# Optimization experiments

Hardware: AMD Instinct MI355X
Metric: run time of the kernel (lower is better)

Reference implementation:

```python
import jax, jax.numpy as jnp
import numpy as np

NUM_USERS = 50000
NUM_ITEMS = 50000
NUM_NODES = NUM_USERS + NUM_ITEMS
EMB_DIM = 128
NUM_LAYERS = 3
NUM_EDGES = 2000000
AVG_DEG = NUM_EDGES / NUM_NODES  # ~20, used to normalize edge weights


def setup_inputs() -> dict:
    key = jax.random.key(0)
    k1, k2, k3, k4 = jax.random.split(key, 4)
    # Xavier-uniform-ish embedding init
    emb_weight = jax.random.normal(k1, (NUM_NODES, EMB_DIM), dtype=jnp.float32) * (1.0 / np.sqrt(EMB_DIM))
    rows = jax.random.randint(k2, (NUM_EDGES,), 0, NUM_NODES, dtype=jnp.int32)
    cols = jax.random.randint(k3, (NUM_EDGES,), 0, NUM_NODES, dtype=jnp.int32)
    # positive normalized edge weights, ~1/deg so spectral radius stays ~1
    vals = jax.random.uniform(k4, (NUM_EDGES,), dtype=jnp.float32) * jnp.float32(2.0 / AVG_DEG)
    return {"emb_weight": emb_weight, "rows": rows, "cols": cols, "vals": vals}


def reference(emb_weight, rows, cols, vals):
    # LightGCN.get_user_item_emb(): multi-layer SpMM propagation + layer mean.
    N = emb_weight.shape[0]

    def spmm(x):
        # out[r] += vals[e] * x[cols[e]] for each edge e with rows[e] == r
        return jax.ops.segment_sum(vals[:, None] * x[cols], rows, num_segments=N)

    x = emb_weight
    acc = x  # running sum of layer outputs (fused stack+mean)
    for _ in range(NUM_LAYERS):
        x = spmm(x)
        acc = acc + x
    x_final = acc / jnp.float32(NUM_LAYERS + 1)
    user_emb = x_final[:NUM_USERS]
    item_emb = x_final[NUM_USERS:]
    return user_emb, item_emb
```

## Files before the change

### kernel.cpp

```cpp
#include <hip/hip_runtime.h>
#include <hip/hip_fp16.h>


#define DIM  128
#define PB   256
#define KPAD 512
#define RPB  256
#define NSCAN (KPAD * PB)
#define NTILES (NSCAN / 1024)
#define PCAP 7168

static inline size_t align_up(size_t v, size_t a) { return (v + a - 1) & ~(a - 1); }

union H2 { unsigned u; __half2 h; };

__global__ void __launch_bounds__(1024)
lgcn_prep(const float2* __restrict__ emb2, int* __restrict__ x0q,
          float* __restrict__ sc0, int n,
          const int* __restrict__ rows, int* __restrict__ ghist, int nedges,
          unsigned long long* __restrict__ tstat) {
    __shared__ int h[KPAD];
    const int b = blockIdx.x, tid = threadIdx.x;
    if (b < PB) {
        for (int k = tid; k < KPAD; k += 1024) h[k] = 0;
        __syncthreads();
        const int chunk = (nedges + PB - 1) / PB;
        const int beg = b * chunk;
        const int end = min(beg + chunk, nedges);
        for (int e = beg + tid; e < end; e += 1024)
            atomicAdd(&h[rows[e] >> 8], 1);
        __syncthreads();
        for (int k = tid; k < KPAD; k += 1024) ghist[(k << 8) + b] = h[k];
    } else if (b == PB) {
        if (tid < NTILES) tstat[tid] = 0ull;
    } else {
        const int wid  = tid >> 6;
        const int lane = tid & 63;
        const int row  = (b - PB - 1) * 16 + wid;
        if (row >= n) return;
        float2 v = emb2[(size_t)row * 64 + lane];
        float m = fmaxf(fabsf(v.x), fabsf(v.y));
        #pragma unroll
        for (int off = 1; off < 64; off <<= 1)
            m = fmaxf(m, __shfl_xor(m, off));
        const float inv = 127.0f / fmaxf(m, 1e-20f);
        int q0 = (int)(v.x * inv + 128.5f);
        int q1 = (int)(v.y * inv + 128.5f);
        q0 = min(max(q0, 0), 255); q1 = min(max(q1, 0), 255);
        ((unsigned short*)x0q)[(size_t)row * 64 + lane] =
            (unsigned short)(q0 | (q1 << 8));
        if (lane == 0) sc0[row] = m * (1.0f / 127.0f);
    }
}

__global__ void __launch_bounds__(256)
lgcn_scan(const int* __restrict__ ghist, int* __restrict__ gbase,
          unsigned long long* __restrict__ tstat, int nscan) {
    __shared__ int wsum[4];
    __shared__ int btot_s, prev_s;
    const int tile = blockIdx.x;
    const int tid  = threadIdx.x;
    const int lane = tid & 63;
    const int wid  = tid >> 6;
    const int i0   = tile * 1024 + tid * 4;

    int4 c = *(const int4*)(ghist + i0);
    const int t1 = c.x + c.y, t2 = t1 + c.z, tsum = t2 + c.w;

    int incl = tsum;
    #pragma unroll
    for (int off = 1; off < 64; off <<= 1) {
        int t = __shfl_up(incl, off, 64);
        if (lane >= off) incl += t;
    }
    if (lane == 63) wsum[wid] = incl;
    __syncthreads();
    int woff = 0;
    #pragma unroll
    for (int w = 0; w < 4; ++w) woff += (w < wid) ? wsum[w] : 0;
    const int ex = woff + incl - tsum;
    if (tid == 255) btot_s = woff + incl;
    __syncthreads();
    const int btot = btot_s;

    if (tile == 0) {
        if (tid == 0) {
            __hip_atomic_store(&tstat[0],
                (((unsigned long long)(unsigned)btot) << 32) | 2ull,
                __ATOMIC_RELEASE, __HIP_MEMORY_SCOPE_AGENT);
            prev_s = 0;
        }
    } else if (wid == 0) {
        if (lane == 0)
            __hip_atomic_store(&tstat[tile],
                (((unsigned long long)(unsigned)btot) << 32) | 1ull,
                __ATOMIC_RELEASE, __HIP_MEMORY_SCOPE_AGENT);
        int run = 0;
        int base_p = tile - 1;
        while (true) {
            const int p = base_p - lane;
            unsigned long long st;
            if (p >= 0) {
                do {
                    st = __hip_atomic_load(&tstat[p],
                        __ATOMIC_ACQUIRE, __HIP_MEMORY_SCOPE_AGENT);
                    if (((unsigned)st & 3u) != 0u) break;
                    __builtin_amdgcn_s_sleep(1);
                } while (true);
            } else {
                st = 2ull;
            }
            const unsigned f = (unsigned)st & 3u;
            const int v = (int)(unsigned)(st >> 32);
            const unsigned long long inc_mask = __ballot(f == 2u);
            int contrib;
            if (inc_mask != 0ull) {
                const int l_star = (int)(__ffsll((long long)inc_mask) - 1);
                contrib = (lane <= l_star) ? v : 0;
            } else {
                contrib = v;
            }
            #pragma unroll
            for (int off = 1; off < 64; off <<= 1)
                contrib += __shfl_xor(contrib, off);
            run += contrib;
            if (inc_mask != 0ull) break;
            base_p -= 64;
        }
        if (lane == 0) {
            __hip_atomic_store(&tstat[tile],
                (((unsigned long long)(unsigned)(run + btot)) << 32) | 2ull,
                __ATOMIC_RELEASE, __HIP_MEMORY_SCOPE_AGENT);
            prev_s = run;
        }
    }
    __syncthreads();
    const int pv = prev_s;

    int4 o;
    o.x = pv + ex;
    o.y = pv + ex + c.x;
    o.z = pv + ex + t1;
    o.w = pv + ex + t2;
    *(int4*)(gbase + i0) = o;
    if (tile == gridDim.x - 1 && tid == 255) gbase[nscan] = pv + btot;
}

__global__ void __launch_bounds__(1024)
lgcn_part(const int* __restrict__ rows, const int* __restrict__ cols,
          const float* __restrict__ vals, const int* __restrict__ gbase,
          int2* __restrict__ staging, int nedges) {
    __shared__ int lcnt[KPAD];
    const int b = blockIdx.x, tid = threadIdx.x;
    for (int k = tid; k < KPAD; k += 1024) lcnt[k] = gbase[(k << 8) + b];
    __syncthreads();
    const int chunk = (nedges + PB - 1) / PB;
    const int beg = b * chunk;
    const int end = min(beg + chunk, nedges);
    for (int e = beg + tid; e < end; e += 1024) {
        int r   = rows[e];
        int pos = atomicAdd(&lcnt[r >> 8], 1);
        staging[pos] = make_int2(cols[e] | ((r & 255) << 17),
                                 __float_as_int(vals[e] * 256.0f));
    }
}

__global__ void __launch_bounds__(1024)
lgcn_place(const int* __restrict__ gbase, const int2* __restrict__ staging,
           int* __restrict__ row_ptr, int2* __restrict__ edges, int n, int nbuck) {
    __shared__ int rcnt[RPB];
    __shared__ int cur[RPB];
    __shared__ int wsum[4];
    __shared__ int2 cache[PCAP];
    const int k    = blockIdx.x;
    const int tid  = threadIdx.x;
    const int base = gbase[k << 8];
    const int next = gbase[(k + 1) << 8];
    const int cnt  = next - base;
    const bool fit = (cnt <= PCAP);

    if (tid < RPB) rcnt[tid] = 0;
    __syncthreads();
    if (fit) {
        for (int i = tid; i < cnt; i += 1024) {
            int2 p = staging[base + i];
            cache[i] = p;
            atomicAdd(&rcnt[(p.x >> 17) & 255], 1);
        }
    } else {
        for (int i = base + tid; i < next; i += 1024)
            atomicAdd(&rcnt[(staging[i].x >> 17) & 255], 1);
    }
    __syncthreads();

    if (tid < RPB) {
        const int lane = tid & 63;
        const int wid  = tid >> 6;
        const int v = rcnt[tid];
        int incl = v;
        #pragma unroll
        for (int off = 1; off < 64; off <<= 1) {
            int t = __shfl_up(incl, off, 64);
            if (lane >= off) incl += t;
        }
        if (lane == 63) wsum[wid] = incl;
        __syncthreads();
        int woff = 0;
        #pragma unroll
        for (int w = 0; w < 4; ++w) woff += (w < wid) ? wsum[w] : 0;
        const int ex = woff + incl - v;

        cur[tid] = base + ex;
        const int r = (k << 8) + tid;
        if (r < n) row_ptr[r] = base + ex;
        if (k == nbuck - 1 && tid == 0) row_ptr[n] = next;
    } else {
        __syncthreads();
    }
    __syncthreads();

    if (fit) {
        for (int i = tid; i < cnt; i += 1024) {
            int2 p  = cache[i];
            int pos = atomicAdd(&cur[(p.x >> 17) & 255], 1);
            edges[pos] = make_int2(p.x & 0x1FFFF, p.y);
        }
    } else {
        for (int i = base + tid; i < next; i += 1024) {
            int2 p  = staging[i];
            int pos = atomicAdd(&cur[(p.x >> 17) & 255], 1);
            edges[pos] = make_int2(p.x & 0x1FFFF, p.y);
        }
    }
}

__global__ void __launch_bounds__(256)
lgcn_spmm(const int* __restrict__ row_ptr, const int2* __restrict__ edges,
          const int2* __restrict__ xq, const float* __restrict__ scin,
          int2* __restrict__ xqout, float* __restrict__ scout,
          const float2* __restrict__ emb, const int2* __restrict__ x1q,
          const float* __restrict__ sc1, float2* __restrict__ out,
          int n, int mode) {
    const int wave = blockIdx.x * 4 + (threadIdx.x >> 6);
    const int lane = threadIdx.x & 63;
    const int g    = lane >> 4;
    const int l    = lane & 15;
    if (wave >= n) return;
    const int beg = row_ptr[wave];
    const int end = row_ptr[wave + 1];

    H2 A0, A1, A2, A3;
    A0.u = 0; A1.u = 0; A2.u = 0; A3.u = 0;
    H2 BIAS; BIAS.u = 0xE480E480;

#define QFMA8(QQ, SV)                                                         \
    {                                                                         \
        H2 hv; hv.h = __float2half2_rn(SV);                                   \
        H2 p;                                                                 \
        p.u = __builtin_amdgcn_perm(0x64646464u, (unsigned)(QQ).x, 0x05010400u); \
        A0.h = __hfma2(__hadd2(p.h, BIAS.h), hv.h, A0.h);                     \
        p.u = __builtin_amdgcn_perm(0x64646464u, (unsigned)(QQ).x, 0x05030402u); \
        A1.h = __hfma2(__hadd2(p.h, BIAS.h), hv.h, A1.h);                     \
        p.u = __builtin_amdgcn_perm(0x64646464u, (unsigned)(QQ).y, 0x05010400u); \
        A2.h = __hfma2(__hadd2(p.h, BIAS.h), hv.h, A2.h);                     \
        p.u = __builtin_amdgcn_perm(0x64646464u, (unsigned)(QQ).y, 0x05030402u); \
        A3.h = __hfma2(__hadd2(p.h, BIAS.h), hv.h, A3.h);                     \
    }

    int e = beg;
    for (; e + 16 <= end; e += 16) {
        int2 d0 = edges[e + g];
        int2 d1 = edges[e + 4 + g];
        int2 d2 = edges[e + 8 + g];
        int2 d3 = edges[e + 12 + g];
        float s0 = scin[d0.x], s1 = scin[d1.x], s2 = scin[d2.x], s3 = scin[d3.x];
        int2 q0 = xq[d0.x * 16 + l];
        int2 q1 = xq[d1.x * 16 + l];
        int2 q2 = xq[d2.x * 16 + l];
        int2 q3 = xq[d3.x * 16 + l];
        QFMA8(q0, s0 * __int_as_float(d0.y));
        QFMA8(q1, s1 * __int_as_float(d1.y));
        QFMA8(q2, s2 * __int_as_float(d2.y));
        QFMA8(q3, s3 * __int_as_float(d3.y));
    }
    for (; e + 8 <= end; e += 8) {
        int2 d0 = edges[e + g];
        int2 d1 = edges[e + 4 + g];
        float s0 = scin[d0.x], s1 = scin[d1.x];
        int2 q0 = xq[d0.x * 16 + l];
        int2 q1 = xq[d1.x * 16 + l];
        QFMA8(q0, s0 * __int_as_float(d0.y));
        QFMA8(q1, s1 * __int_as_float(d1.y));
    }
    for (; e < end; e += 4) {
        const int ee = e + g;
        int2 d = (ee < end) ? edges[ee] : make_int2(0, 0);
        float s = scin[d.x];
        int2 q = xq[d.x * 16 + l];
        QFMA8(q, s * __int_as_float(d.y));
    }
#undef QFMA8

    const float DS = 0.00390625f;
    float2 f0 = __half22float2(A0.h), f1 = __half22float2(A1.h);
    float2 f2 = __half22float2(A2.h), f3 = __half22float2(A3.h);
    float a0 = f0.x * DS, a1 = f0.y * DS, a2 = f1.x * DS, a3 = f1.y * DS;
    float a4 = f2.x * DS, a5 = f2.y * DS, a6 = f3.x * DS, a7 = f3.y * DS;

    a0 += __shfl_xor(a0, 16); a0 += __shfl_xor(a0, 32);
    a1 += __shfl_xor(a1, 16); a1 += __shfl_xor(a1, 32);
    a2 += __shfl_xor(a2, 16); a2 += __shfl_xor(a2, 32);
    a3 += __shfl_xor(a3, 16); a3 += __shfl_xor(a3, 32);
    a4 += __shfl_xor(a4, 16); a4 += __shfl_xor(a4, 32);
    a5 += __shfl_xor(a5, 16); a5 += __shfl_xor(a5, 32);
    a6 += __shfl_xor(a6, 16); a6 += __shfl_xor(a6, 32);
    a7 += __shfl_xor(a7, 16); a7 += __shfl_xor(a7, 32);

    if (mode == 0) {
        float m = fmaxf(fmaxf(fmaxf(fabsf(a0), fabsf(a1)), fmaxf(fabsf(a2), fabsf(a3))),
                        fmaxf(fmaxf(fabsf(a4), fabsf(a5)), fmaxf(fabsf(a6), fabsf(a7))));
        m = fmaxf(m, __shfl_xor(m, 1));
        m = fmaxf(m, __shfl_xor(m, 2));
        m = fmaxf(m, __shfl_xor(m, 4));
        m = fmaxf(m, __shfl_xor(m, 8));
        const float inv = 127.0f / fmaxf(m, 1e-20f);
        int q0 = min(max((int)(a0 * inv + 128.5f), 0), 255);
        int q1 = min(max((int)(a1 * inv + 128.5f), 0), 255);
        int q2 = min(max((int)(a2 * inv + 128.5f), 0), 255);
        int q3 = min(max((int)(a3 * inv + 128.5f), 0), 255);
        int q4 = min(max((int)(a4 * inv + 128.5f), 0), 255);
        int q5 = min(max((int)(a5 * inv + 128.5f), 0), 255);
        int q6 = min(max((int)(a6 * inv + 128.5f), 0), 255);
        int q7 = min(max((int)(a7 * inv + 128.5f), 0), 255);
        if (g == 0) {
            int2 r;
            r.x = q0 | (q1 << 8) | (q2 << 16) | (q3 << 24);
            r.y = q4 | (q5 << 8) | (q6 << 16) | (q7 << 24);
            xqout[wave * 16 + l] = r;
            if (l == 0) scout[wave] = m * (1.0f / 127.0f);
        }
    } else {
        if (g == 0) {
            float4 e0 = ((const float4*)emb)[wave * 32 + l * 2 + 0];
            float4 e1 = ((const float4*)emb)[wave * 32 + l * 2 + 1];
            int2 u1 = x1q[wave * 16 + l];
            int2 u2 = xq[wave * 16 + l];
            const float s1 = sc1[wave],  o1 = -128.0f * s1;
            const float s2 = scin[wave], o2 = -128.0f * s2;
            float b0 = fmaf((float)( u1.x        & 255), s1, o1);
            float b1 = fmaf((float)((u1.x >> 8)  & 255), s1, o1);
            float b2 = fmaf((float)((u1.x >> 16) & 255), s1, o1);
            float b3 = fmaf((float)((u1.x >> 24) & 255), s1, o1);
            float b4 = fmaf((float)( u1.y        & 255), s1, o1);
            float b5 = fmaf((float)((u1.y >> 8)  & 255), s1, o1);
            float b6 = fmaf((float)((u1.y >> 16) & 255), s1, o1);
            float b7 = fmaf((float)((u1.y >> 24) & 255), s1, o1);
            float c0 = fmaf((float)( u2.x        & 255), s2, o2);
            float c1 = fmaf((float)((u2.x >> 8)  & 255), s2, o2);
            float c2 = fmaf((float)((u2.x >> 16) & 255), s2, o2);
            float c3 = fmaf((float)((u2.x >> 24) & 255), s2, o2);
            float c4 = fmaf((float)( u2.y        & 255), s2, o2);
            float c5 = fmaf((float)((u2.y >> 8)  & 255), s2, o2);
            float c6 = fmaf((float)((u2.y >> 16) & 255), s2, o2);
            float c7 = fmaf((float)((u2.y >> 24) & 255), s2, o2);
            float4 r0, r1;
            r0.x = (e0.x + b0 + c0 + a0) * 0.25f;
            r0.y = (e0.y + b1 + c1 + a1) * 0.25f;
            r0.z = (e0.z + b2 + c2 + a2) * 0.25f;
            r0.w = (e0.w + b3 + c3 + a3) * 0.25f;
            r1.x = (e1.x + b4 + c4 + a4) * 0.25f;
            r1.y = (e1.y + b5 + c5 + a5) * 0.25f;
            r1.z = (e1.z + b6 + c6 + a6) * 0.25f;
            r1.w = (e1.w + b7 + c7 + a7) * 0.25f;
            ((float4*)out)[wave * 32 + l * 2 + 0] = r0;
            ((float4*)out)[wave * 32 + l * 2 + 1] = r1;
        }
    }
}

extern "C" void kernel_launch(void* const* d_in, const int* in_sizes, int n_in,
                              void* d_out, int out_size, void* d_ws, size_t ws_size,
                              hipStream_t stream) {
    const float* emb  = (const float*)d_in[0];
    const int*   rows = (const int*)d_in[1];
    const int*   cols = (const int*)d_in[2];
    const float* vals = (const float*)d_in[3];

    const int  n_nodes = in_sizes[0] / DIM;
    const int  nedges  = in_sizes[1];
    const long nd      = (long)n_nodes * DIM;

    char* ws = (char*)d_ws;
    size_t off = 0;
    int2* bufA    = (int2*)(ws + off); off = align_up(off + (size_t)nd, 256);
    int2* bufB    = (int2*)(ws + off); off = align_up(off + (size_t)nd, 256);
    int2* edges   = (int2*)(ws + off); off = align_up(off + (size_t)nedges * 8, 256);
    int2* staging = (int2*)(ws + off); off = align_up(off + (size_t)nedges * 8, 256);
    float* scA    = (float*)(ws + off); off = align_up(off + (size_t)n_nodes * 4, 256);
    float* scB    = (float*)(ws + off); off = align_up(off + (size_t)n_nodes * 4, 256);
    int* row_ptr  = (int*)(ws + off);  off = align_up(off + (size_t)(n_nodes + 1) * 4, 256);
    int* ghist    = (int*)(ws + off);  off = align_up(off + (size_t)NSCAN * 4, 256);
    int* gbase    = (int*)(ws + off);  off = align_up(off + ((size_t)NSCAN + 1) * 4, 256);
    unsigned long long* tstat = (unsigned long long*)(ws + off);
    off = align_up(off + (size_t)NTILES * 8, 256);
    float2* out   = (float2*)d_out;

    const int BS = 256;
    const int nbuck   = (n_nodes + RPB - 1) / RPB;
    const int grid_c  = (n_nodes + 15) / 16;
    const int grid_s  = (n_nodes + 3) / 4;

    lgcn_prep<<<PB + 1 + grid_c, 1024, 0, stream>>>((const float2*)emb, (int*)bufA,
                                                    scA, n_nodes, rows, ghist,
                                                    nedges, tstat);
    lgcn_scan<<<NTILES, BS, 0, stream>>>(ghist, gbase, tstat, NSCAN);
    lgcn_part<<<PB, 1024, 0, stream>>>(rows, cols, vals, gbase, staging, nedges);
    lgcn_place<<<nbuck, 1024, 0, stream>>>(gbase, staging, row_ptr, edges, n_nodes, nbuck);

    lgcn_spmm<<<grid_s, BS, 0, stream>>>(row_ptr, edges, bufA, scA, bufB, scB,
                                         nullptr, nullptr, nullptr, nullptr,
                                         n_nodes, 0);
    lgcn_spmm<<<grid_s, BS, 0, stream>>>(row_ptr, edges, bufB, scB, bufA, scA,
                                         nullptr, nullptr, nullptr, nullptr,
                                         n_nodes, 0);
    lgcn_spmm<<<grid_s, BS, 0, stream>>>(row_ptr, edges, bufA, scA, nullptr, nullptr,
                                         (const float2*)emb, bufB, scB, out,
                                         n_nodes, 1);
}
```

Measured before the change: 356.0 us.

## Fuse graph-build kernels into one persistent kernel with grid barriers

Merges the prep, scan, partition and place kernels into a single persistent 256-block kernel that separates phases with atomic grid-wide barriers. The decoupled-lookback scan becomes a two-level scan: per-tile scans, a single-block scan of tile sums, then an add pass. The goal is to remove the launch overheads and tail gaps between the build kernels. In exchange it adds five global barriers and depends on all 256 blocks of 1024 threads being co-resident; if they are not, the kernel deadlocks. It also loses parallelism in the quantize and place phases, since fixed blocks now loop over that work.

Measured after the change: 452.3 us. +27.1%, slower.

```diff
diff --git a/kernel.cpp b/kernel.cpp
--- a/kernel.cpp
+++ b/kernel.cpp
@@ -9,194 +9,76 @@
 #define NSCAN (KPAD * PB)
 #define NTILES (NSCAN / 1024)
 #define PCAP 7168
+#define NB   256
+#define NT   1024
 
 static inline size_t align_up(size_t v, size_t a) { return (v + a - 1) & ~(a - 1); }
 
 union H2 { unsigned u; __half2 h; };
 
+__device__ __forceinline__ void gbar(int* bar, int target) {
+    __syncthreads();
+    if (threadIdx.x == 0) {
+        __hip_atomic_fetch_add(bar, 1, __ATOMIC_ACQ_REL, __HIP_MEMORY_SCOPE_AGENT);
+        while (__hip_atomic_load(bar, __ATOMIC_ACQUIRE,
+                                 __HIP_MEMORY_SCOPE_AGENT) < target)
+            __builtin_amdgcn_s_sleep(2);
+    }
+    __syncthreads();
+}
+
 __global__ void __launch_bounds__(1024)
-lgcn_prep(const float2* __restrict__ emb2, int* __restrict__ x0q,
-          float* __restrict__ sc0, int n,
-          const int* __restrict__ rows, int* __restrict__ ghist, int nedges,
-          unsigned long long* __restrict__ tstat) {
-    __shared__ int h[KPAD];
-    const int b = blockIdx.x, tid = threadIdx.x;
-    if (b < PB) {
-        for (int k = tid; k < KPAD; k += 1024) h[k] = 0;
-        __syncthreads();
-        const int chunk = (nedges + PB - 1) / PB;
-        const int beg = b * chunk;
-        const int end = min(beg + chunk, nedges);
-        for (int e = beg + tid; e < end; e += 1024)
-            atomicAdd(&h[rows[e] >> 8], 1);
-        __syncthreads();
-        for (int k = tid; k < KPAD; k += 1024) ghist[(k << 8) + b] = h[k];
-    } else if (b == PB) {
-        if (tid < NTILES) tstat[tid] = 0ull;
-    } else {
-        const int wid  = tid >> 6;
-        const int lane = tid & 63;
-        const int row  = (b - PB - 1) * 16 + wid;
-        if (row >= n) return;
-        float2 v = emb2[(size_t)row * 64 + lane];
-        float m = fmaxf(fabsf(v.x), fabsf(v.y));
-        #pragma unroll
-        for (int off = 1; off < 64; off <<= 1)
-            m = fmaxf(m, __shfl_xor(m, off));
-        const float inv = 127.0f / fmaxf(m, 1e-20f);
-        int q0 = (int)(v.x * inv + 128.5f);
-        int q1 = (int)(v.y * inv + 128.5f);
-        q0 = min(max(q0, 0), 255); q1 = min(max(q1, 0), 255);
-        ((unsigned short*)x0q)[(size_t)row * 64 + lane] =
-            (unsigned short)(q0 | (q1 << 8));
-        if (lane == 0) sc0[row] = m * (1.0f / 127.0f);
-    }
-}
-
-__global__ void __launch_bounds__(256)
-lgcn_scan(const int* __restrict__ ghist, int* __restrict__ gbase,
-          unsigned long long* __restrict__ tstat, int nscan) {
-    __shared__ int wsum[4];
-    __shared__ int btot_s, prev_s;
-    const int tile = blockIdx.x;
+lgcn_build(const float2* __restrict__ emb2, int* __restrict__ x0q,
+           float* __restrict__ sc0, int n,
+           const int* __restrict__ rows, const int* __restrict__ cols,
+           const float* __restrict__ vals,
+           int* __restrict__ ghist, int* __restrict__ gbase,
+           int* __restrict__ bsums, int2* __restrict__ staging,
+           int2* __restrict__ edges, int* __restrict__ row_ptr,
+           int nedges, int nbuck, int* __restrict__ bar) {
+    __shared__ int2 cache[PCAP];
+    __shared__ int  hh[KPAD];
+    __shared__ int  rcnt[RPB];
+    __shared__ int  cur[RPB];
+    __shared__ int  wsum[16];
+    __shared__ int  wext[17];
+
+    const int b    = blockIdx.x;
     const int tid  = threadIdx.x;
     const int lane = tid & 63;
     const int wid  = tid >> 6;
-    const int i0   = tile * 1024 + tid * 4;
-
-    int4 c = *(const int4*)(ghist + i0);
-    const int t1 = c.x + c.y, t2 = t1 + c.z, tsum = t2 + c.w;
-
-    int incl = tsum;
-    #pragma unroll
-    for (int off = 1; off < 64; off <<= 1) {
-        int t = __shfl_up(incl, off, 64);
-        if (lane >= off) incl += t;
-    }
-    if (lane == 63) wsum[wid] = incl;
-    __syncthreads();
-    int woff = 0;
-    #pragma unroll
-    for (int w = 0; w < 4; ++w) woff += (w < wid) ? wsum[w] : 0;
-    const int ex = woff + incl - tsum;
-    if (tid == 255) btot_s = woff + incl;
-    __syncthreads();
-    const int btot = btot_s;
-
-    if (tile == 0) {
-        if (tid == 0) {
-            __hip_atomic_store(&tstat[0],
-                (((unsigned long long)(unsigned)btot) << 32) | 2ull,
-                __ATOMIC_RELEASE, __HIP_MEMORY_SCOPE_AGENT);
-            prev_s = 0;
-        }
-    } else if (wid == 0) {
-        if (lane == 0)
-            __hip_atomic_store(&tstat[tile],
-                (((unsigned long long)(unsigned)btot) << 32) | 1ull,
-                __ATOMIC_RELEASE, __HIP_MEMORY_SCOPE_AGENT);
-        int run = 0;
-        int base_p = tile - 1;
-        while (true) {
-            const int p = base_p - lane;
-            unsigned long long st;
-            if (p >= 0) {
-                do {
-                    st = __hip_atomic_load(&tstat[p],
-                        __ATOMIC_ACQUIRE, __HIP_MEMORY_SCOPE_AGENT);
-                    if (((unsigned)st & 3u) != 0u) break;
-                    __builtin_amdgcn_s_sleep(1);
-                } while (true);
-            } else {
-                st = 2ull;
-            }
-            const unsigned f = (unsigned)st & 3u;
-            const int v = (int)(unsigned)(st >> 32);
-            const unsigned long long inc_mask = __ballot(f == 2u);
-            int contrib;
-            if (inc_mask != 0ull) {
-                const int l_star = (int)(__ffsll((long long)inc_mask) - 1);
-                contrib = (lane <= l_star) ? v : 0;
-            } else {
-                contrib = v;
-            }
-            #pragma unroll
-            for (int off = 1; off < 64; off <<= 1)
-                contrib += __shfl_xor(contrib, off);
-            run += contrib;
-            if (inc_mask != 0ull) break;
-            base_p -= 64;
-        }
-        if (lane == 0) {
-            __hip_atomic_store(&tstat[tile],
-                (((unsigned long long)(unsigned)(run + btot)) << 32) | 2ull,
-                __ATOMIC_RELEASE, __HIP_MEMORY_SCOPE_AGENT);
-            prev_s = run;
-        }
-    }
-    __syncthreads();
-    const int pv = prev_s;
-
-    int4 o;
-    o.x = pv + ex;
-    o.y = pv + ex + c.x;
-    o.z = pv + ex + t1;
-    o.w = pv + ex + t2;
-    *(int4*)(gbase + i0) = o;
-    if (tile == gridDim.x - 1 && tid == 255) gbase[nscan] = pv + btot;
-}
-
-__global__ void __launch_bounds__(1024)
-lgcn_part(const int* __restrict__ rows, const int* __restrict__ cols,
-          const float* __restrict__ vals, const int* __restrict__ gbase,
-          int2* __restrict__ staging, int nedges) {
-    __shared__ int lcnt[KPAD];
-    const int b = blockIdx.x, tid = threadIdx.x;
-    for (int k = tid; k < KPAD; k += 1024) lcnt[k] = gbase[(k << 8) + b];
-    __syncthreads();
     const int chunk = (nedges + PB - 1) / PB;
     const int beg = b * chunk;
     const int end = min(beg + chunk, nedges);
-    for (int e = beg + tid; e < end; e += 1024) {
-        int r   = rows[e];
-        int pos = atomicAdd(&lcnt[r >> 8], 1);
-        staging[pos] = make_int2(cols[e] | ((r & 255) << 17),
-                                 __float_as_int(vals[e] * 256.0f));
-    }
-}
-
-__global__ void __launch_bounds__(1024)
-lgcn_place(const int* __restrict__ gbase, const int2* __restrict__ staging,
-           int* __restrict__ row_ptr, int2* __restrict__ edges, int n, int nbuck) {
-    __shared__ int rcnt[RPB];
-    __shared__ int cur[RPB];
-    __shared__ int wsum[4];
-    __shared__ int2 cache[PCAP];
-    const int k    = blockIdx.x;
-    const int tid  = threadIdx.x;
-    const int base = gbase[k << 8];
-    const int next = gbase[(k + 1) << 8];
-    const int cnt  = next - base;
-    const bool fit = (cnt <= PCAP);
-
-    if (tid < RPB) rcnt[tid] = 0;
-    __syncthreads();
-    if (fit) {
-        for (int i = tid; i < cnt; i += 1024) {
-            int2 p = staging[base + i];
-            cache[i] = p;
-            atomicAdd(&rcnt[(p.x >> 17) & 255], 1);
-        }
-    } else {
-        for (int i = base + tid; i < next; i += 1024)
-            atomicAdd(&rcnt[(staging[i].x >> 17) & 255], 1);
-    }
-    __syncthreads();
-
-    if (tid < RPB) {
-        const int lane = tid & 63;
-        const int wid  = tid >> 6;
-        const int v = rcnt[tid];
+
+    for (int k = tid; k < KPAD; k += NT) hh[k] = 0;
+    __syncthreads();
+    for (int e = beg + tid; e < end; e += NT)
+        atomicAdd(&hh[rows[e] >> 8], 1);
+    const int ngrp = (n + 15) >> 4;
+    for (int grp = b; grp < ngrp; grp += NB) {
+        const int row = grp * 16 + wid;
+        if (row < n) {
+            float2 v = emb2[(size_t)row * 64 + lane];
+            float m = fmaxf(fabsf(v.x), fabsf(v.y));
+            #pragma unroll
+            for (int off = 1; off < 64; off <<= 1)
+                m = fmaxf(m, __shfl_xor(m, off));
+            const float inv = 127.0f / fmaxf(m, 1e-20f);
+            int q0 = min(max((int)(v.x * inv + 128.5f), 0), 255);
+            int q1 = min(max((int)(v.y * inv + 128.5f), 0), 255);
+            ((unsigned short*)x0q)[(size_t)row * 64 + lane] =
+                (unsigned short)(q0 | (q1 << 8));
+            if (lane == 0) sc0[row] = m * (1.0f / 127.0f);
+        }
+    }
+    __syncthreads();
+    for (int k = tid; k < KPAD; k += NT) ghist[(k << 8) + b] = hh[k];
+    gbar(bar, NB * 1);
+
+    if (b < NTILES) {
+        const int i0 = b * 1024 + tid;
+        const int v = ghist[i0];
         int incl = v;
         #pragma unroll
         for (int off = 1; off < 64; off <<= 1) {
@@ -205,32 +87,107 @@
         }
         if (lane == 63) wsum[wid] = incl;
         __syncthreads();
-        int woff = 0;
+        if (tid == 0) {
+            int r = 0;
+            #pragma unroll
+            for (int w = 0; w < 16; ++w) { wext[w] = r; r += wsum[w]; }
+            wext[16] = r;
+        }
+        __syncthreads();
+        gbase[i0] = wext[wid] + incl - v;
+        if (tid == 0) bsums[b] = wext[16];
+    }
+    gbar(bar, NB * 2);
+
+    if (b == 0) {
+        int v = (tid < NTILES) ? bsums[tid] : 0;
+        int incl = v;
         #pragma unroll
-        for (int w = 0; w < 4; ++w) woff += (w < wid) ? wsum[w] : 0;
-        const int ex = woff + incl - v;
-
-        cur[tid] = base + ex;
-        const int r = (k << 8) + tid;
-        if (r < n) row_ptr[r] = base + ex;
-        if (k == nbuck - 1 && tid == 0) row_ptr[n] = next;
-    } else {
-        __syncthreads();
-    }
-    __syncthreads();
-
-    if (fit) {
-        for (int i = tid; i < cnt; i += 1024) {
-            int2 p  = cache[i];
-            int pos = atomicAdd(&cur[(p.x >> 17) & 255], 1);
-            edges[pos] = make_int2(p.x & 0x1FFFF, p.y);
-        }
-    } else {
-        for (int i = base + tid; i < next; i += 1024) {
-            int2 p  = staging[i];
-            int pos = atomicAdd(&cur[(p.x >> 17) & 255], 1);
-            edges[pos] = make_int2(p.x & 0x1FFFF, p.y);
-        }
+        for (int off = 1; off < 64; off <<= 1) {
+            int t = __shfl_up(incl, off, 64);
+            if (lane >= off) incl += t;
+        }
+        if (tid == 63) wsum[0] = incl;
+        __syncthreads();
+        if (tid < NTILES) {
+            const int ex = incl - v + ((wid == 1) ? wsum[0] : 0);
+            bsums[tid] = ex;
+            if (tid == NTILES - 1) gbase[NSCAN] = ex + v;
+        }
+    }
+    gbar(bar, NB * 3);
+
+    {
+        const int i = b * 1024 + tid;
+        if (i < NSCAN) gbase[i] += bsums[i >> 10];
+    }
+    gbar(bar, NB * 4);
+
+    for (int k = tid; k < KPAD; k += NT) hh[k] = gbase[(k << 8) + b];
+    __syncthreads();
+    for (int e = beg + tid; e < end; e += NT) {
+        int r   = rows[e];
+        int pos = atomicAdd(&hh[r >> 8], 1);
+        staging[pos] = make_int2(cols[e] | ((r & 255) << 17),
+                                 __float_as_int(vals[e] * 256.0f));
+    }
+    gbar(bar, NB * 5);
+
+    for (int k = b; k < nbuck; k += NB) {
+        const int base = gbase[k << 8];
+        const int next = gbase[(k + 1) << 8];
+        const int cnt  = next - base;
+        const bool fit = (cnt <= PCAP);
+
+        if (tid < RPB) rcnt[tid] = 0;
+        __syncthreads();
+        if (fit) {
+            for (int i = tid; i < cnt; i += NT) {
+                int2 p = staging[base + i];
+                cache[i] = p;
+                atomicAdd(&rcnt[(p.x >> 17) & 255], 1);
+            }
+        } else {
+            for (int i = base + tid; i < next; i += NT)
+                atomicAdd(&rcnt[(staging[i].x >> 17) & 255], 1);
+        }
+        __syncthreads();
+
+        int v = (tid < RPB) ? rcnt[tid] : 0;
+        int incl = v;
+        #pragma unroll
+        for (int off = 1; off < 64; off <<= 1) {
+            int t = __shfl_up(incl, off, 64);
+            if (lane >= off) incl += t;
+        }
+        if (wid < 4 && lane == 63) wsum[wid] = incl;
+        __syncthreads();
+        if (tid < RPB) {
+            int woff = 0;
+            #pragma unroll
+            for (int w = 0; w < 4; ++w) woff += (w < wid) ? wsum[w] : 0;
+            const int ex = woff + incl - v;
+            cur[tid] = base + ex;
+            const int r = (k << 8) + tid;
+            if (r < n) row_ptr[r] = base + ex;
+            if (k == nbuck - 1 && tid == 0) row_ptr[n] = next;
+        }
+        __syncthreads();
+
+        if (fit) {
+            for (int i = tid; i < cnt; i += NT) {
+                int2 p  = cache[i];
+                int pos = atomicAdd(&cur[(p.x >> 17) & 255], 1);
+                edges[pos] = make_int2(p.x & 0x1FFFF, p.y);
+            }
+        } else {
+            for (int i = base + tid; i < next; i += NT) {
+                int2 p  = staging[i];
+                int pos = atomicAdd(&cur[(p.x >> 17) & 255], 1);
+                edges[pos] = make_int2(p.x & 0x1FFFF, p.y);
+            }
+        }
+        __syncthreads();
     }
 }
 
@@ -401,21 +358,18 @@
     int* row_ptr  = (int*)(ws + off);  off = align_up(off + (size_t)(n_nodes + 1) * 4, 256);
     int* ghist    = (int*)(ws + off);  off = align_up(off + (size_t)NSCAN * 4, 256);
     int* gbase    = (int*)(ws + off);  off = align_up(off + ((size_t)NSCAN + 1) * 4, 256);
-    unsigned long long* tstat = (unsigned long long*)(ws + off);
-    off = align_up(off + (size_t)NTILES * 8, 256);
+    int* bsums    = (int*)(ws + off);  off = align_up(off + (size_t)NTILES * 4, 256);
+    int* bar      = (int*)(ws + off);  off = align_up(off + 256, 256);
     float2* out   = (float2*)d_out;
 
     const int BS = 256;
-    const int nbuck   = (n_nodes + RPB - 1) / RPB;
-    const int grid_c  = (n_nodes + 15) / 16;
-    const int grid_s  = (n_nodes + 3) / 4;
-
-    lgcn_prep<<<PB + 1 + grid_c, 1024, 0, stream>>>((const float2*)emb, (int*)bufA,
-                                                    scA, n_nodes, rows, ghist,
-                                                    nedges, tstat);
-    lgcn_scan<<<NTILES, BS, 0, stream>>>(ghist, gbase, tstat, NSCAN);
-    lgcn_part<<<PB, 1024, 0, stream>>>(rows, cols, vals, gbase, staging, nedges);
-    lgcn_place<<<nbuck, 1024, 0, stream>>>(gbase, staging, row_ptr, edges, n_nodes, nbuck);
+    const int nbuck  = (n_nodes + RPB - 1) / RPB;
+    const int grid_s = (n_nodes + 3) / 4;
+
+    hipMemsetAsync(bar, 0, sizeof(int), stream);
+    lgcn_build<<<NB, NT, 0, stream>>>((const float2*)emb, (int*)bufA, scA, n_nodes,
+                                      rows, cols, vals, ghist, gbase, bsums,
+                                      staging, edges, row_ptr, nedges, nbuck, bar);
 
     lgcn_spmm<<<grid_s, BS, 0, stream>>>(row_ptr, edges, bufA, scA, bufB, scB,
                                          nullptr, nullptr, nullptr, nullptr,
```

## Requantize embeddings to per-bucket scales held in LDS for SpMM gathers

Applied to the files above, without the earlier changes.

Adds a rescale pass that converts per-row int8 quantization scales into one shared scale per 256-row bucket, re-encoding each row's bytes. The SpMM kernel then loads all bucket scales into LDS and reads the gather scale from there instead of doing a random global load per edge. The first rescale is folded into the partition kernel as extra blocks, and SpMM moves to 1024-thread blocks. This adds two extra rescale launches and loses precision for rows whose magnitude is far below the bucket maximum.

New measurement: 408.7 us. 14.8% more time.

```diff
diff --git a/kernel.cpp b/kernel.cpp
--- a/kernel.cpp
+++ b/kernel.cpp
@@ -44,9 +44,8 @@
         for (int off = 1; off < 64; off <<= 1)
             m = fmaxf(m, __shfl_xor(m, off));
         const float inv = 127.0f / fmaxf(m, 1e-20f);
-        int q0 = (int)(v.x * inv + 128.5f);
-        int q1 = (int)(v.y * inv + 128.5f);
-        q0 = min(max(q0, 0), 255); q1 = min(max(q1, 0), 255);
+        int q0 = min(max((int)(v.x * inv + 128.5f), 0), 255);
+        int q1 = min(max((int)(v.y * inv + 128.5f), 0), 255);
         ((unsigned short*)x0q)[(size_t)row * 64 + lane] =
             (unsigned short)(q0 | (q1 << 8));
         if (lane == 0) sc0[row] = m * (1.0f / 127.0f);
@@ -146,22 +145,85 @@
     if (tile == gridDim.x - 1 && tid == 255) gbase[nscan] = pv + btot;
 }
 
+__device__ __forceinline__ void rescale_bucket(int k, int* __restrict__ xq,
+                                               const float* __restrict__ scR,
+                                               float* __restrict__ sB, int n,
+                                               float* srow, float* smax) {
+    const int tid = threadIdx.x;
+    const int rbeg = k << 8;
+    if (tid < RPB) {
+        int r = rbeg + tid;
+        srow[tid] = (r < n) ? scR[r] : 0.f;
+    }
+    __syncthreads();
+    if (tid < RPB) {
+        float v = srow[tid];
+        #pragma unroll
+        for (int off = 1; off < 64; off <<= 1) v = fmaxf(v, __shfl_xor(v, off));
+        if ((tid & 63) == 0) smax[tid >> 6] = v;
+    }
+    __syncthreads();
+    const float sBv = fmaxf(fmaxf(fmaxf(smax[0], smax[1]),
+                                  fmaxf(smax[2], smax[3])), 1e-20f);
+    if (tid == 0) sB[k] = sBv;
+    const int row = rbeg + (tid >> 2);
+    if (row >= n) return;
+    const float ratio = srow[tid >> 2] / sBv;
+    int4* p = (int4*)xq + (size_t)row * 8 + (size_t)(tid & 3) * 2;
+    #pragma unroll
+    for (int h = 0; h < 2; ++h) {
+        int4 v = p[h];
+        int r0 = v.x, r1 = v.y, r2 = v.z, r3 = v.w;
+        int o0 = 0, o1 = 0, o2 = 0, o3 = 0;
+        #pragma unroll
+        for (int byt = 0; byt < 4; ++byt) {
+            int b0 = (r0 >> (byt * 8)) & 255;
+            int b1 = (r1 >> (byt * 8)) & 255;
+            int b2 = (r2 >> (byt * 8)) & 255;
+            int b3 = (r3 >> (byt * 8)) & 255;
+            int n0 = min(max((int)(((float)b0 - 128.f) * ratio + 128.5f), 0), 255);
+            int n1 = min(max((int)(((float)b1 - 128.f) * ratio + 128.5f), 0), 255);
+            int n2 = min(max((int)(((float)b2 - 128.f) * ratio + 128.5f), 0), 255);
+            int n3 = min(max((int)(((float)b3 - 128.f) * ratio + 128.5f), 0), 255);
+            o0 |= n0 << (byt * 8); o1 |= n1 << (byt * 8);
+            o2 |= n2 << (byt * 8); o3 |= n3 << (byt * 8);
+        }
+        p[h] = make_int4(o0, o1, o2, o3);
+    }
+}
+
+__global__ void __launch_bounds__(1024)
+lgcn_rescale(int* __restrict__ xq, const float* __restrict__ scR,
+             float* __restrict__ sB, int n) {
+    __shared__ float srow[RPB];
+    __shared__ float smax[4];
+    rescale_bucket(blockIdx.x, xq, scR, sB, n, srow, smax);
+}
+
 __global__ void __launch_bounds__(1024)
 lgcn_part(const int* __restrict__ rows, const int* __restrict__ cols,
           const float* __restrict__ vals, const int* __restrict__ gbase,
-          int2* __restrict__ staging, int nedges) {
+          int2* __restrict__ staging, int nedges,
+          int* __restrict__ x0q, const float* __restrict__ scR,
+          float* __restrict__ sB0, int n) {
     __shared__ int lcnt[KPAD];
+    __shared__ float srow[RPB];
+    __shared__ float smax[4];
     const int b = blockIdx.x, tid = threadIdx.x;
-    for (int k = tid; k < KPAD; k += 1024) lcnt[k] = gbase[(k << 8) + b];
-    __syncthreads();
-    const int chunk = (nedges + PB - 1) / PB;
-    const int beg = b * chunk;
-    const int end = min(beg + chunk, nedges);
-    for (int e = beg + tid; e < end; e += 1024) {
-        int r   = rows[e];
-        int pos = atomicAdd(&lcnt[r >> 8], 1);
-        staging[pos] = make_int2(cols[e] | ((r & 255) << 17),
-                                 __float_as_int(vals[e] * 256.0f));
+    if (b < PB) {
+        for (int k = tid; k < KPAD; k += 1024) lcnt[k] = gbase[(k << 8) + b];
+        __syncthreads();
+        const int chunk = (nedges + PB - 1) / PB;
+        const int beg = b * chunk;
+        const int end = min(beg + chunk, nedges);
+        for (int e = beg + tid; e < end; e += 1024) {
+            int r   = rows[e];
+            int pos = atomicAdd(&lcnt[r >> 8], 1);
+            staging[pos] = make_int2(cols[e] | ((r & 255) << 17),
+                                     __float_as_int(vals[e] * 256.0f));
+        }
+    } else {
+        rescale_bucket(b - PB, x0q, scR, sB0, n, srow, smax);
     }
 }
 
@@ -213,7 +275,7 @@
         cur[tid] = base + ex;
         const int r = (k << 8) + tid;
         if (r < n) row_ptr[r] = base + ex;
-        if (k == nbuck - 1 && tid == 0) row_ptr[n] = next;
+        if (k == gridDim.x - 1 && tid == 0) row_ptr[n] = next;
     } else {
         __syncthreads();
     }
@@ -234,15 +296,24 @@
     }
 }
 
-__global__ void __launch_bounds__(256)
+__global__ void __launch_bounds__(1024)
 lgcn_spmm(const int* __restrict__ row_ptr, const int2* __restrict__ edges,
-          const int2* __restrict__ xq, const float* __restrict__ scin,
+          const int2* __restrict__ xq, const float* __restrict__ sBin,
           int2* __restrict__ xqout, float* __restrict__ scout,
           const float2* __restrict__ emb, const int2* __restrict__ x1q,
-          const float* __restrict__ sc1, float2* __restrict__ out,
+          const float* __restrict__ sB1, float2* __restrict__ out,
           int n, int mode) {
-    const int wave = blockIdx.x * 4 + (threadIdx.x >> 6);
-    const int lane = threadIdx.x & 63;
+    __shared__ float lsc[KPAD];
+    __shared__ float lsc1[KPAD];
+    const int tid = threadIdx.x;
+    for (int i = tid; i < KPAD; i += 1024) {
+        lsc[i] = sBin[i];
+        if (mode != 0) lsc1[i] = sB1[i];
+    }
+    __syncthreads();
+
+    const int wave = blockIdx.x * 16 + (tid >> 6);
+    const int lane = tid & 63;
     const int g    = lane >> 4;
     const int l    = lane & 15;
     if (wave >= n) return;
@@ -273,7 +344,8 @@
         int2 d1 = edges[e + 4 + g];
         int2 d2 = edges[e + 8 + g];
         int2 d3 = edges[e + 12 + g];
-        float s0 = scin[d0.x], s1 = scin[d1.x], s2 = scin[d2.x], s3 = scin[d3.x];
+        float s0 = lsc[d0.x >> 8], s1 = lsc[d1.x >> 8];
+        float s2 = lsc[d2.x >> 8], s3 = lsc[d3.x >> 8];
         int2 q0 = xq[d0.x * 16 + l];
         int2 q1 = xq[d1.x * 16 + l];
         int2 q2 = xq[d2.x * 16 + l];
@@ -286,7 +358,7 @@
     for (; e + 8 <= end; e += 8) {
         int2 d0 = edges[e + g];
         int2 d1 = edges[e + 4 + g];
-        float s0 = scin[d0.x], s1 = scin[d1.x];
+        float s0 = lsc[d0.x >> 8], s1 = lsc[d1.x >> 8];
         int2 q0 = xq[d0.x * 16 + l];
         int2 q1 = xq[d1.x * 16 + l];
         QFMA8(q0, s0 * __int_as_float(d0.y));
@@ -295,7 +367,7 @@
     for (; e < end; e += 4) {
         const int ee = e + g;
         int2 d = (ee < end) ? edges[ee] : make_int2(0, 0);
-        float s = scin[d.x];
+        float s = lsc[d.x >> 8];
         int2 q = xq[d.x * 16 + l];
         QFMA8(q, s * __int_as_float(d.y));
     }
@@ -345,8 +417,8 @@
             float4 e1 = ((const float4*)emb)[wave * 32 + l * 2 + 1];
             int2 u1 = x1q[wave * 16 + l];
             int2 u2 = xq[wave * 16 + l];
-            const float s1 = sc1[wave],  o1 = -128.0f * s1;
-            const float s2 = scin[wave], o2 = -128.0f * s2;
+            const float s1 = lsc1[wave >> 8], o1 = -128.0f * s1;
+            const float s2 = lsc[wave >> 8],  o2 = -128.0f * s2;
             float b0 = fmaf((float)( u1.x        & 255), s1, o1);
             float b1 = fmaf((float)((u1.x >> 8)  & 255), s1, o1);
             float b2 = fmaf((float)((u1.x >> 16) & 255), s1, o1);
@@ -398,6 +470,9 @@
     int2* staging = (int2*)(ws + off); off = align_up(off + (size_t)nedges * 8, 256);
     float* scA    = (float*)(ws + off); off = align_up(off + (size_t)n_nodes * 4, 256);
     float* scB    = (float*)(ws + off); off = align_up(off + (size_t)n_nodes * 4, 256);
+    float* sB0    = (float*)(ws + off); off = align_up(off + (size_t)KPAD * 4, 256);
+    float* sB1    = (float*)(ws + off); off = align_up(off + (size_t)KPAD * 4, 256);
+    float* sB2    = (float*)(ws + off); off = align_up(off + (size_t)KPAD * 4, 256);
     int* row_ptr  = (int*)(ws + off);  off = align_up(off + (size_t)(n_nodes + 1) * 4, 256);
     int* ghist    = (int*)(ws + off);  off = align_up(off + (size_t)NSCAN * 4, 256);
     int* gbase    = (int*)(ws + off);  off = align_up(off + ((size_t)NSCAN + 1) * 4, 256);
@@ -405,25 +480,28 @@
     off = align_up(off + (size_t)NTILES * 8, 256);
     float2* out   = (float2*)d_out;
 
-    const int BS = 256;
     const int nbuck   = (n_nodes + RPB - 1) / RPB;
     const int grid_c  = (n_nodes + 15) / 16;
-    const int grid_s  = (n_nodes + 3) / 4;
+    const int grid_s  = (n_nodes + 15) / 16;
 
     lgcn_prep<<<PB + 1 + grid_c, 1024, 0, stream>>>((const float2*)emb, (int*)bufA,
                                                     scA, n_nodes, rows, ghist,
                                                     nedges, tstat);
-    lgcn_scan<<<NTILES, BS, 0, stream>>>(ghist, gbase, tstat, NSCAN);
-    lgcn_part<<<PB, 1024, 0, stream>>>(rows, cols, vals, gbase, staging, nedges);
-    lgcn_place<<<nbuck, 1024, 0, stream>>>(gbase, staging, row_ptr, edges, n_nodes, nbuck);
-
-    lgcn_spmm<<<grid_s, BS, 0, stream>>>(row_ptr, edges, bufA, scA, bufB, scB,
-                                         nullptr, nullptr, nullptr, nullptr,
-                                         n_nodes, 0);
-    lgcn_spmm<<<grid_s, BS, 0, stream>>>(row_ptr, edges, bufB, scB, bufA, scA,
-                                         nullptr, nullptr, nullptr, nullptr,
-                                         n_nodes, 0);
-    lgcn_spmm<<<grid_s, BS, 0, stream>>>(row_ptr, edges, bufA, scA, nullptr, nullptr,
-                                         (const float2*)emb, bufB, scB, out,
-                                         n_nodes, 1);
-}
+    lgcn_scan<<<NTILES, 256, 0, stream>>>(ghist, gbase, tstat, NSCAN);
+    lgcn_part<<<PB + nbuck, 1024, 0, stream>>>(rows, cols, vals, gbase, staging,
+                                               nedges, (int*)bufA, scA, sB0, n_nodes);
+    lgcn_place<<<nbuck, 1024, 0, stream>>>(gbase, staging, row_ptr, edges,
+                                           n_nodes, nbuck);
+
+    lgcn_spmm<<<grid_s, 1024, 0, stream>>>(row_ptr, edges, bufA, sB0, bufB, scB,
+                                           nullptr, nullptr, nullptr, nullptr,
+                                           n_nodes, 0);
+    lgcn_rescale<<<nbuck, 1024, 0, stream>>>((int*)bufB, scB, sB1, n_nodes);
+    lgcn_spmm<<<grid_s, 1024, 0, stream>>>(row_ptr, edges, bufB, sB1, bufA, scA,
+                                           nullptr, nullptr, nullptr, nullptr,
+                                           n_nodes, 0);
+    lgcn_rescale<<<nbuck, 1024, 0, stream>>>((int*)bufA, scA, sB2, n_nodes);
+    lgcn_spmm<<<grid_s, 1024, 0, stream>>>(row_ptr, edges, bufA, sB2, nullptr,
+                                           nullptr, (const float2*)emb, bufB,
+                                           sB1, out, n_nodes, 1);
+}
```
